# Kernel tuning notes

Hardware: AMD Instinct MI355X
Metric: run time of the kernel (lower is better)

## Reference

```python
import jax, jax.numpy as jnp
import numpy as np

B, H, W = 8, 48, 48
D_MODEL, D_STATE, SSM_RATIO, K = 192, 16, 2.0, 4
D_INNER = int(SSM_RATIO * D_MODEL)        # 384
DT_RANK = int(np.ceil(D_MODEL / 16))       # 12
EPS = 1e-6


def setup_inputs() -> dict:
    key = jax.random.key(0)
    ks = jax.random.split(key, 12)
    s = 0.02
    inp = {
        "x": jax.random.normal(ks[0], (B, H, W, D_MODEL), jnp.float32),
        "in_proj_w": s * jax.random.normal(ks[1], (2 * D_INNER, D_MODEL), jnp.float32),
        "conv_w": s * jax.random.normal(ks[2], (D_INNER, 1, 3, 3), jnp.float32),
        "conv_b": jnp.zeros((D_INNER,), jnp.float32),
        "x_proj_w": s * jax.random.normal(ks[3], (K, DT_RANK + 2 * D_STATE, D_INNER), jnp.float32),
        "dt_w": s * jax.random.normal(ks[4], (K, D_INNER, DT_RANK), jnp.float32),
        "dt_bias": 0.05 * jax.random.normal(ks[5], (K, D_INNER), jnp.float32),
        "A_logs": jnp.log(jnp.broadcast_to(jnp.arange(1, D_STATE + 1, dtype=jnp.float32), (K * D_INNER, D_STATE)).copy()),
        "Ds": jnp.ones((K * D_INNER,), jnp.float32),
        "ln_w": jnp.ones((D_INNER,), jnp.float32),
        "ln_b": jnp.zeros((D_INNER,), jnp.float32),
        "out_proj_w": s * jax.random.normal(ks[6], (D_MODEL, D_INNER), jnp.float32),
    }
    return inp


def _selective_scan(u, dt, A, Bs, Cs):
    # u, dt: (B,K,D,L); A: (K,D,N); Bs, Cs: (B,K,N,L)
    u_t = jnp.moveaxis(u, -1, 0)    # (L,B,K,D)
    dt_t = jnp.moveaxis(dt, -1, 0)  # (L,B,K,D)
    B_t = jnp.moveaxis(Bs, -1, 0)   # (L,B,K,N)
    C_t = jnp.moveaxis(Cs, -1, 0)   # (L,B,K,N)
    b = u.shape[0]
    h0 = jnp.zeros((b, K, D_INNER, D_STATE), jnp.float32)

    def step(h, inp):
        ut, dtt, bt, ct = inp
        dA = jnp.exp(dtt[..., None] * A)                       # (B,K,D,N)
        h = dA * h + (dtt * ut)[..., None] * bt[:, :, None, :]  # (B,K,D,N)
        y = jnp.einsum('bkdn,bkn->bkd', h, ct)
        return h, y

    _, ys = jax.lax.scan(step, h0, (u_t, dt_t, B_t, C_t))
    return jnp.moveaxis(ys, 0, -1)  # (B,K,D,L)


def reference(x, in_proj_w, conv_w, conv_b, x_proj_w, dt_w, dt_bias, A_logs, Ds, ln_w, ln_b, out_proj_w):
    b, h, w, _ = x.shape
    L = h * w
    # in_proj + split into x / gate z
    xz = jnp.einsum('bhwc,oc->bhwo', x, in_proj_w)
    xi, z = jnp.split(xz, 2, axis=-1)
    z = jax.nn.silu(z)
    # depthwise 3x3 conv, channel-first
    xi = jnp.transpose(xi, (0, 3, 1, 2))  # (B,Di,H,W)
    xi = jax.lax.conv_general_dilated(
        xi, conv_w, window_strides=(1, 1), padding='SAME',
        feature_group_count=D_INNER,
        dimension_numbers=('NCHW', 'OIHW', 'NCHW')) + conv_b[None, :, None, None]
    xi = jax.nn.silu(xi)
    # cross-scan: 4 directions (row-major, col-major, and their reverses)
    xr = xi.reshape(b, D_INNER, L)
    xc = jnp.transpose(xi, (0, 1, 3, 2)).reshape(b, D_INNER, L)
    xs = jnp.stack([xr, xc, jnp.flip(xr, -1), jnp.flip(xc, -1)], axis=1)  # (B,K,D,L)
    # per-direction projections
    x_dbl = jnp.einsum('bkdl,kcd->bkcl', xs, x_proj_w)  # (B,K,R+2N,L)
    dts = x_dbl[:, :, :DT_RANK]
    Bs = x_dbl[:, :, DT_RANK:DT_RANK + D_STATE]
    Cs = x_dbl[:, :, DT_RANK + D_STATE:]
    dts = jnp.einsum('bkrl,kdr->bkdl', dts, dt_w)
    A = -jnp.exp(A_logs.astype(jnp.float32)).reshape(K, D_INNER, D_STATE)
    dt = jax.nn.softplus(dts + dt_bias[None, :, :, None])
    ys = _selective_scan(xs.astype(jnp.float32), dt, A, Bs.astype(jnp.float32), Cs.astype(jnp.float32))
    ys = ys + Ds.reshape(1, K, D_INNER, 1) * xs  # skip
    # cross-merge (invert each direction, sum)
    def col2row(t):
        return jnp.transpose(t.reshape(b, D_INNER, w, h), (0, 1, 3, 2)).reshape(b, D_INNER, L)
    y = ys[:, 0] + col2row(ys[:, 1]) + jnp.flip(ys[:, 2], -1) + col2row(jnp.flip(ys[:, 3], -1))
    y = jnp.transpose(y.reshape(b, D_INNER, h, w), (0, 2, 3, 1))  # (B,H,W,Di)
    # LayerNorm over channel dim
    mu = y.mean(-1, keepdims=True)
    var = ((y - mu) ** 2).mean(-1, keepdims=True)
    y = (y - mu) / jnp.sqrt(var + EPS) * ln_w + ln_b
    # gate + out_proj
    y = y * z
    out = jnp.einsum('bhwd,od->bhwo', y, out_proj_w)
    return out.astype(x.dtype)
```

## Files before the change

kernel.cpp:

```cpp
#include <hip/hip_runtime.h>

#define BB 8
#define HH 48
#define WW2 48
#define LL 2304
#define CIN 192
#define DI 384
#define NK 4
#define RR 12
#define NS 16
#define CD 44
#define NX 176
#define MM 18432
#define NC 48
#define CL 48

typedef unsigned short u16;
typedef __attribute__((ext_vector_type(8))) short s16x8;
typedef __attribute__((ext_vector_type(4))) float f32x4;

static __device__ __forceinline__ float siluf(float x) { return x / (1.f + __expf(-x)); }

static __device__ __forceinline__ u16 f2bf(float x) {
    unsigned u = __float_as_uint(x);
    return (u16)((u + 0x7FFFu + ((u >> 16) & 1u)) >> 16);
}
static __device__ __forceinline__ float bf2f(u16 h) {
    return __uint_as_float(((unsigned)h) << 16);
}

static __device__ __forceinline__ int posmap(int k, int l) {
    switch (k & 3) {
    case 0: return l;
    case 1: { int w = l / HH; int h = l - w * HH; return h * WW2 + w; }
    case 2: return LL - 1 - l;
    default: { int j = LL - 1 - l; int w = j / HH; int h = j - w * HH; return h * WW2 + w; }
    }
}

__global__ __launch_bounds__(256) void k_cvt2(const float* __restrict__ in,
                                              u16* __restrict__ hi,
                                              u16* __restrict__ lo, int n) {
    int i = (blockIdx.x * 256 + threadIdx.x) * 4;
    if (i >= n) return;
    float4 v = *(const float4*)(in + i);
    u16 h0 = f2bf(v.x), h1 = f2bf(v.y), h2 = f2bf(v.z), h3 = f2bf(v.w);
    hi[i + 0] = h0; hi[i + 1] = h1; hi[i + 2] = h2; hi[i + 3] = h3;
    lo[i + 0] = f2bf(v.x - bf2f(h0));
    lo[i + 1] = f2bf(v.y - bf2f(h1));
    lo[i + 2] = f2bf(v.z - bf2f(h2));
    lo[i + 3] = f2bf(v.w - bf2f(h3));
}

template<int N, int K, int EPI>
__global__ __launch_bounds__(256) void k_gemm(const u16* __restrict__ Ahg,
                                              const u16* __restrict__ Alg,
                                              const u16* __restrict__ Bhg,
                                              const u16* __restrict__ Blg,
                                              float* __restrict__ O1,
                                              void* __restrict__ O2) {
    __shared__ __align__(16) u16 lds[12288];
    const int m0 = blockIdx.x << 7;
    const int n0 = blockIdx.y << 6;
    const int t = threadIdx.x;
    const int lane = t & 63;
    const int w = t >> 6;
    const int wm = w & 1, wn = w >> 1;

    f32x4 acc[4][2];
#pragma unroll
    for (int mi = 0; mi < 4; ++mi)
#pragma unroll
        for (int ni = 0; ni < 2; ++ni)
#pragma unroll
            for (int r = 0; r < 4; ++r) acc[mi][ni][r] = 0.f;

    const int rA = lane & 15;
    const int kb = (lane >> 4) << 3;

    for (int k0 = 0; k0 < K; k0 += 32) {
#pragma unroll
        for (int rep = 0; rep < 2; ++rep) {
            int q = t + (rep << 8);
            int row = q >> 2;
            int kk = (q & 3) << 3;
            size_t ga = (size_t)(m0 + row) * K + k0 + kk;
            *(uint4*)&lds[(row << 5) + kk] = *(const uint4*)(Ahg + ga);
            *(uint4*)&lds[4096 + (row << 5) + kk] = *(const uint4*)(Alg + ga);
        }
        {
            int row = t >> 2;
            int kk = (t & 3) << 3;
            int rg = n0 + row;
            if (N & 63) rg = (rg > N - 1) ? (N - 1) : rg;
            size_t gb = (size_t)rg * K + k0 + kk;
            *(uint4*)&lds[8192 + (row << 5) + kk] = *(const uint4*)(Bhg + gb);
            *(uint4*)&lds[10240 + (row << 5) + kk] = *(const uint4*)(Blg + gb);
        }
        __syncthreads();

        s16x8 bh[2], bl[2];
#pragma unroll
        for (int ni = 0; ni < 2; ++ni) {
            int c = (wn << 5) + (ni << 4) + rA;
            bh[ni] = *(const s16x8*)&lds[8192 + (c << 5) + kb];
            bl[ni] = *(const s16x8*)&lds[10240 + (c << 5) + kb];
        }
#pragma unroll
        for (int mi = 0; mi < 4; ++mi) {
            int rr = (wm << 6) + (mi << 4) + rA;
            s16x8 ah = *(const s16x8*)&lds[(rr << 5) + kb];
            s16x8 al = *(const s16x8*)&lds[4096 + (rr << 5) + kb];
#pragma unroll
            for (int ni = 0; ni < 2; ++ni) {
                acc[mi][ni] = __builtin_amdgcn_mfma_f32_16x16x32_bf16(al, bh[ni], acc[mi][ni], 0, 0, 0);
                acc[mi][ni] = __builtin_amdgcn_mfma_f32_16x16x32_bf16(ah, bl[ni], acc[mi][ni], 0, 0, 0);
                acc[mi][ni] = __builtin_amdgcn_mfma_f32_16x16x32_bf16(ah, bh[ni], acc[mi][ni], 0, 0, 0);
            }
        }
        __syncthreads();
    }

    const int rbase = (lane >> 4) << 2;
#pragma unroll
    for (int mi = 0; mi < 4; ++mi) {
#pragma unroll
        for (int ni = 0; ni < 2; ++ni) {
            int o = n0 + (wn << 5) + (ni << 4) + (lane & 15);
#pragma unroll
            for (int r = 0; r < 4; ++r) {
                int m = m0 + (wm << 6) + (mi << 4) + rbase + r;
                float v = acc[mi][ni][r];
                if (EPI == 0) {
                    if (o < DI) O1[(size_t)m * DI + o] = v;
                    else        ((u16*)O2)[(size_t)m * DI + (o - DI)] = f2bf(siluf(v));
                } else if (EPI == 1) {
                    if (o < NX) O1[(size_t)m * NX + o] = v;
                } else {
                    O1[(size_t)m * CIN + o] = v;
                }
            }
        }
    }
}

__global__ __launch_bounds__(128) void k_conv(const float* __restrict__ xi,
                                              const float* __restrict__ cw,
                                              const float* __restrict__ cb,
                                              float* __restrict__ ub,
                                              u16* __restrict__ ubh,
                                              u16* __restrict__ ubl) {
    int blk = blockIdx.x;
    int b = blk / LL, p = blk - b * LL;
    int h = p / WW2, w = p - h * WW2;
    for (int d = threadIdx.x; d < DI; d += 128) {
        float acc = cb[d];
#pragma unroll
        for (int dh = -1; dh <= 1; ++dh) {
            int hh = h + dh;
            if (hh < 0 || hh >= HH) continue;
#pragma unroll
            for (int dw = -1; dw <= 1; ++dw) {
                int ww = w + dw;
                if (ww < 0 || ww >= WW2) continue;
                acc = fmaf(cw[d * 9 + (dh + 1) * 3 + (dw + 1)],
                           xi[((size_t)b * LL + hh * WW2 + ww) * DI + d], acc);
            }
        }
        float o = siluf(acc);
        size_t idx = ((size_t)b * LL + p) * DI + d;
        ub[idx] = o;
        u16 hh2 = f2bf(o);
        ubh[idx] = hh2;
        ubl[idx] = f2bf(o - bf2f(hh2));
    }
}

static __device__ __forceinline__ void adv_p(int k, int& p, int& hh) {
    if (k == 0) { ++p; }
    else if (k == 2) { --p; }
    else if (k == 1) {
        bool wrap = (hh == HH - 1);
        hh = wrap ? 0 : hh + 1;
        p += wrap ? -(LL - 1 - HH) : WW2;
    } else {
        bool wrap = (hh == 0);
        hh = wrap ? HH - 1 : hh - 1;
        p += wrap ? (LL - 1 - HH) : -WW2;
    }
}

static __device__ __forceinline__ void init_p(int k, int l0, int& p, int& hh) {
    hh = 0;
    if (k == 0) p = l0;
    else if (k == 2) p = LL - 1 - l0;
    else if (k == 1) { int w0 = l0 / HH; hh = l0 - w0 * HH; p = hh * WW2 + w0; }
    else { int j0 = LL - 1 - l0; int w0 = j0 / HH; hh = j0 - w0 * HH; p = hh * WW2 + w0; }
}

static __device__ __forceinline__ void scan_decode(int blk, int& b, int& k, int& dblk, int& c) {
    b = blk & 7;
    int r = blk >> 3;
    c = r % NC;
    int t2 = r / NC;
    dblk = t2 % 3;
    k = t2 / 3;
}

__global__ __launch_bounds__(128) void k_scan1(const float* __restrict__ ub,
                                               const float* __restrict__ xdbl,
                                               const float* __restrict__ dt_w,
                                               const float* __restrict__ dt_bias,
                                               const float* __restrict__ A_logs,
                                               float* __restrict__ HF,
                                               float* __restrict__ SD) {
    int b, k, dblk, c;
    scan_decode(blockIdx.x, b, k, dblk, c);
    int bk = (b << 2) | k;
    int d = (dblk << 7) + threadIdx.x;
    int kd = k * DI + d;

    float dtw[RR];
#pragma unroll
    for (int r = 0; r < RR; ++r) dtw[r] = dt_w[(size_t)kd * RR + r];
    float dtb = dt_bias[kd];
    float a[NS];
    bool fast = true;
#pragma unroll
    for (int n = 0; n < NS; ++n) {
        a[n] = -__expf(A_logs[(size_t)kd * NS + n]);
        fast = fast && (fabsf(a[n] + (float)(n + 1)) < 1e-3f * (float)(n + 1));
    }
    int use_fast = __all((int)fast);

    float h[NS];
#pragma unroll
    for (int n = 0; n < NS; ++n) h[n] = 0.f;
    float sumdt = 0.f;

    const float* cb0 = xdbl + (size_t)b * LL * NX + k * CD;
    const float* ubase = ub + (size_t)b * LL * DI + d;
    const int l0 = c * CL;
    int p, hh;
    init_p(k, l0, p, hh);

    if (use_fast) {
        for (int li = 0; li < CL; ++li) {
            const float4* cp4 = (const float4*)(cb0 + (size_t)p * NX);
            float dq[12];
            *(float4*)(dq + 0) = cp4[0];
            *(float4*)(dq + 4) = cp4[1];
            *(float4*)(dq + 8) = cp4[2];
            float s = dtb;
#pragma unroll
            for (int r = 0; r < RR; ++r) s = fmaf(dtw[r], dq[r], s);
            float es = __expf(s);
            float dt = (s > 15.f) ? s : __logf(1.f + es);
            float E = __builtin_amdgcn_rcpf(1.f + es);
            sumdt += dt;
            float uv = ubase[(size_t)p * DI];
            float du = dt * uv;
            float bb2[16];
            *(float4*)(bb2 + 0)  = cp4[3];
            *(float4*)(bb2 + 4)  = cp4[4];
            *(float4*)(bb2 + 8)  = cp4[5];
            *(float4*)(bb2 + 12) = cp4[6];
            float pw = 1.f;
#pragma unroll
            for (int n = 0; n < NS; ++n) {
                pw *= E;
                h[n] = fmaf(du, bb2[n], pw * h[n]);
            }
            adv_p(k, p, hh);
        }
    } else {
        for (int li = 0; li < CL; ++li) {
            int l = l0 + li;
            int pp = posmap(k, l);
            const float* cp = cb0 + (size_t)pp * NX;
            float s = dtb;
#pragma unroll
            for (int r = 0; r < RR; ++r) s = fmaf(dtw[r], cp[r], s);
            float dt = (s > 15.f) ? s : log1pf(__expf(s));
            sumdt += dt;
            float uv = ubase[(size_t)pp * DI];
            float du = dt * uv;
#pragma unroll
            for (int n = 0; n < NS; ++n) {
                float dA = __expf(dt * a[n]);
                h[n] = fmaf(du, cp[RR + n], dA * h[n]);
            }
        }
    }
    size_t base = ((size_t)bk * NC + c);
#pragma unroll
    for (int n = 0; n < NS; ++n) HF[(base * NS + n) * DI + d] = h[n];
    SD[base * DI + d] = sumdt;
}

__global__ __launch_bounds__(256) void k_scan2(const float* __restrict__ A_logs,
                                               float* __restrict__ HF,
                                               const float* __restrict__ SD) {
    int idx = blockIdx.x * 256 + threadIdx.x;
    int bk = idx / DI;
    int d = idx - bk * DI;
    int k = bk & 3;
    int kd = k * DI + d;

    float a[NS];
    bool fast = true;
#pragma unroll
    for (int n = 0; n < NS; ++n) {
        a[n] = -__expf(A_logs[(size_t)kd * NS + n]);
        fast = fast && (fabsf(a[n] + (float)(n + 1)) < 1e-3f * (float)(n + 1));
    }
    int use_fast = __all((int)fast);

    float H[NS];
#pragma unroll
    for (int n = 0; n < NS; ++n) H[n] = 0.f;

    for (int c = 0; c < NC; ++c) {
        size_t base = ((size_t)bk * NC + c);
        float sd = SD[base * DI + d];
        if (use_fast) {
            float E = __expf(-sd);
            float pw = 1.f;
#pragma unroll
            for (int n = 0; n < NS; ++n) {
                pw *= E;
                float hf = HF[(base * NS + n) * DI + d];
                HF[(base * NS + n) * DI + d] = H[n];
                H[n] = fmaf(pw, H[n], hf);
            }
        } else {
#pragma unroll
            for (int n = 0; n < NS; ++n) {
                float dec = __expf(a[n] * sd);
                float hf = HF[(base * NS + n) * DI + d];
                HF[(base * NS + n) * DI + d] = H[n];
                H[n] = fmaf(dec, H[n], hf);
            }
        }
    }
}

__global__ __launch_bounds__(128) void k_scan3(const float* __restrict__ ub,
                                               const float* __restrict__ xdbl,
                                               const float* __restrict__ dt_w,
                                               const float* __restrict__ dt_bias,
                                               const float* __restrict__ A_logs,
                                               const float* __restrict__ Ds,
                                               const float* __restrict__ HF,
                                               float* __restrict__ ycomb) {
    int b, k, dblk, c;
    scan_decode(blockIdx.x, b, k, dblk, c);
    int bk = (b << 2) | k;
    int d = (dblk << 7) + threadIdx.x;
    int kd = k * DI + d;

    float dtw[RR];
#pragma unroll
    for (int r = 0; r < RR; ++r) dtw[r] = dt_w[(size_t)kd * RR + r];
    float dtb = dt_bias[kd];
    float dsv = Ds[kd];
    float a[NS];
    bool fast = true;
#pragma unroll
    for (int n = 0; n < NS; ++n) {
        a[n] = -__expf(A_logs[(size_t)kd * NS + n]);
        fast = fast && (fabsf(a[n] + (float)(n + 1)) < 1e-3f * (float)(n + 1));
    }
    int use_fast = __all((int)fast);

    float h[NS];
    size_t sbase = ((size_t)bk * NC + c);
#pragma unroll
    for (int n = 0; n < NS; ++n) h[n] = HF[(sbase * NS + n) * DI + d];

    const float* cb0 = xdbl + (size_t)b * LL * NX + k * CD;
    const float* ubase = ub + (size_t)b * LL * DI + d;
    float* ybase = ycomb + (size_t)b * LL * DI + d;
    const int l0 = c * CL;
    int p, hh;
    init_p(k, l0, p, hh);

    if (use_fast) {
        for (int li = 0; li < CL; ++li) {
            const float4* cp4 = (const float4*)(cb0 + (size_t)p * NX);
            float dq[12];
            *(float4*)(dq + 0) = cp4[0];
            *(float4*)(dq + 4) = cp4[1];
            *(float4*)(dq + 8) = cp4[2];
            float s = dtb;
#pragma unroll
            for (int r = 0; r < RR; ++r) s = fmaf(dtw[r], dq[r], s);
            float es = __expf(s);
            float dt = (s > 15.f) ? s : __logf(1.f + es);
            float E = __builtin_amdgcn_rcpf(1.f + es);
            float uv = ubase[(size_t)p * DI];
            float du = dt * uv;
            float bc[32];
            *(float4*)(bc + 0)  = cp4[3];
            *(float4*)(bc + 4)  = cp4[4];
            *(float4*)(bc + 8)  = cp4[5];
            *(float4*)(bc + 12) = cp4[6];
            *(float4*)(bc + 16) = cp4[7];
            *(float4*)(bc + 20) = cp4[8];
            *(float4*)(bc + 24) = cp4[9];
            *(float4*)(bc + 28) = cp4[10];
            float pw = 1.f, y = 0.f;
#pragma unroll
            for (int n = 0; n < NS; ++n) {
                pw *= E;
                h[n] = fmaf(du, bc[n], pw * h[n]);
                y = fmaf(h[n], bc[NS + n], y);
            }
            atomicAdd(ybase + (size_t)p * DI, fmaf(dsv, uv, y));
            adv_p(k, p, hh);
        }
    } else {
        for (int li = 0; li < CL; ++li) {
            int l = l0 + li;
            int pp = posmap(k, l);
            const float* cp = cb0 + (size_t)pp * NX;
            float s = dtb;
#pragma unroll
            for (int r = 0; r < RR; ++r) s = fmaf(dtw[r], cp[r], s);
            float dt = (s > 15.f) ? s : log1pf(__expf(s));
            float uv = ubase[(size_t)pp * DI];
            float du = dt * uv;
            float y = 0.f;
#pragma unroll
            for (int n = 0; n < NS; ++n) {
                float dA = __expf(dt * a[n]);
                h[n] = fmaf(du, cp[RR + n], dA * h[n]);
                y = fmaf(h[n], cp[RR + NS + n], y);
            }
            atomicAdd(ybase + (size_t)pp * DI, fmaf(dsv, uv, y));
        }
    }
}

static __device__ __forceinline__ float waveRedSum(float v) {
#pragma unroll
    for (int o = 32; o; o >>= 1) v += __shfl_down(v, o);
    return v;
}

__global__ __launch_bounds__(128) void k_lngate(const float* __restrict__ ycomb,
                                                const u16* __restrict__ zb16,
                                                const float* __restrict__ lnw,
                                                const float* __restrict__ lnb,
                                                u16* __restrict__ ylnh,
                                                u16* __restrict__ ylnl) {
    int m = blockIdx.x;
    const float* yr = ycomb + (size_t)m * DI;
    float v[3];
    float s1 = 0.f, s2 = 0.f;
#pragma unroll
    for (int i = 0; i < 3; ++i) {
        v[i] = yr[threadIdx.x + (i << 7)];
        s1 += v[i];
        s2 = fmaf(v[i], v[i], s2);
    }
    s1 = waveRedSum(s1);
    s2 = waveRedSum(s2);
    __shared__ float p1[2], p2[2];
    int wid = threadIdx.x >> 6, lane = threadIdx.x & 63;
    if (lane == 0) { p1[wid] = s1; p2[wid] = s2; }
    __syncthreads();
    float S1 = p1[0] + p1[1];
    float S2 = p2[0] + p2[1];
    float mu = S1 * (1.f / DI);
    float var = S2 * (1.f / DI) - mu * mu;
    float rstd = rsqrtf(var + 1e-6f);
#pragma unroll
    for (int i = 0; i < 3; ++i) {
        int dd = threadIdx.x + (i << 7);
        float o = ((v[i] - mu) * rstd) * lnw[dd] + lnb[dd];
        float g = o * bf2f(zb16[(size_t)m * DI + dd]);
        u16 hh = f2bf(g);
        ylnh[(size_t)m * DI + dd] = hh;
        ylnl[(size_t)m * DI + dd] = f2bf(g - bf2f(hh));
    }
}

extern "C" void kernel_launch(void* const* d_in, const int* in_sizes, int n_in,
                              void* d_out, int out_size, void* d_ws, size_t ws_size,
                              hipStream_t stream) {
    const float* x         = (const float*)d_in[0];
    const float* in_proj_w = (const float*)d_in[1];
    const float* conv_w    = (const float*)d_in[2];
    const float* conv_b    = (const float*)d_in[3];
    const float* x_proj_w  = (const float*)d_in[4];
    const float* dt_w      = (const float*)d_in[5];
    const float* dt_bias   = (const float*)d_in[6];
    const float* A_logs    = (const float*)d_in[7];
    const float* Ds        = (const float*)d_in[8];
    const float* ln_w      = (const float*)d_in[9];
    const float* ln_b      = (const float*)d_in[10];
    const float* out_proj_w= (const float*)d_in[11];
    float* out = (float*)d_out;
    float* ws  = (float*)d_ws;

    const size_t SZ = (size_t)MM * DI;
    float* xi    = ws;
    u16*   zb16  = (u16*)(ws + SZ + SZ / 2);
    float* ub    = ws + 2 * SZ;
    float* xdbl  = ws + 3 * SZ;
    float* ycomb = ws + 3 * SZ + (size_t)MM * NX;
    u16*   wpl   = (u16*)(ycomb + SZ);

    u16* wphi  = wpl;
    u16* wplo  = wpl + 147456;
    u16* xpwhi = wpl + 294912;
    u16* xpwlo = wpl + 362496;
    u16* wohi  = wpl + 430080;
    u16* wolo  = wpl + 503808;

    u16* xhi  = (u16*)ub;  u16* xlo  = xhi + (size_t)MM * CIN;
    u16* ubh  = (u16*)ycomb; u16* ubl = ubh + SZ;
    u16* ylnh = (u16*)xi;  u16* ylnl = ylnh + SZ;
    float* HF = ws;
    float* SD = ws + (size_t)BB * NK * NC * NS * DI;

    k_cvt2<<<3456, 256, 0, stream>>>(x, xhi, xlo, MM * CIN);
    k_cvt2<<<144, 256, 0, stream>>>(in_proj_w, wphi, wplo, 768 * CIN);
    k_cvt2<<<66, 256, 0, stream>>>(x_proj_w, xpwhi, xpwlo, NX * DI);
    k_cvt2<<<72, 256, 0, stream>>>(out_proj_w, wohi, wolo, CIN * DI);

    k_gemm<768, CIN, 0><<<dim3(MM / 128, 12), 256, 0, stream>>>(xhi, xlo, wphi, wplo, xi, (void*)zb16);

    k_conv<<<MM, 128, 0, stream>>>(xi, conv_w, conv_b, ub, ubh, ubl);

    k_gemm<NX, DI, 1><<<dim3(MM / 128, 3), 256, 0, stream>>>(ubh, ubl, xpwhi, xpwlo, xdbl, nullptr);

    hipMemsetAsync(ycomb, 0, SZ * sizeof(float), stream);

    const int nscan = BB * NK * 3 * NC;
    k_scan1<<<nscan, 128, 0, stream>>>(ub, xdbl, dt_w, dt_bias, A_logs, HF, SD);
    k_scan2<<<BB * NK * DI / 256, 256, 0, stream>>>(A_logs, HF, SD);
    k_scan3<<<nscan, 128, 0, stream>>>(ub, xdbl, dt_w, dt_bias, A_logs, Ds, HF, ycomb);

    k_lngate<<<MM, 128, 0, stream>>>(ycomb, zb16, ln_w, ln_b, ylnh, ylnl);

    k_gemm<CIN, DI, 2><<<dim3(MM / 128, 3), 256, 0, stream>>>(ylnh, ylnl, wohi, wolo, out, nullptr);
}
```

Before: 368.9 us.

## Fuse x hi/lo bf16 split into in_proj GEMM and widen scan blocks

The in_proj GEMM now loads fp32 x directly and splits it into bf16 hi/lo pairs while staging tiles into LDS. This removes the separate conversion kernel and the round trip of the split copies through global memory. The scan kernels also switch from 128-thread blocks over three channel slices to one 384-thread block covering all channels, cutting the block count threefold. In exchange there is conversion arithmetic inside the GEMM load loop and fewer, larger scan blocks with more register pressure per block.

```diff
diff --git a/kernel.cpp b/kernel.cpp
--- a/kernel.cpp
+++ b/kernel.cpp
@@ -52,7 +52,7 @@
     lo[i + 3] = f2bf(v.w - bf2f(h3));
 }
 
-template<int N, int K, int EPI>
+template<int N, int K, int EPI, int ACVT>
 __global__ __launch_bounds__(256) void k_gemm(const u16* __restrict__ Ahg,
                                               const u16* __restrict__ Alg,
                                               const u16* __restrict__ Bhg,
@@ -85,8 +85,24 @@
             int row = q >> 2;
             int kk = (q & 3) << 3;
             size_t ga = (size_t)(m0 + row) * K + k0 + kk;
-            *(uint4*)&lds[(row << 5) + kk] = *(const uint4*)(Ahg + ga);
-            *(uint4*)&lds[4096 + (row << 5) + kk] = *(const uint4*)(Alg + ga);
+            if (ACVT) {
+                const float* Af = (const float*)Ahg;
+                float vv[8];
+                *(float4*)(vv + 0) = *(const float4*)(Af + ga);
+                *(float4*)(vv + 4) = *(const float4*)(Af + ga + 4);
+                u16 hbuf[8], lbuf[8];
+#pragma unroll
+                for (int i = 0; i < 8; ++i) {
+                    u16 h = f2bf(vv[i]);
+                    hbuf[i] = h;
+                    lbuf[i] = f2bf(vv[i] - bf2f(h));
+                }
+                *(uint4*)&lds[(row << 5) + kk] = *(uint4*)hbuf;
+                *(uint4*)&lds[4096 + (row << 5) + kk] = *(uint4*)lbuf;
+            } else {
+                *(uint4*)&lds[(row << 5) + kk] = *(const uint4*)(Ahg + ga);
+                *(uint4*)&lds[4096 + (row << 5) + kk] = *(const uint4*)(Alg + ga);
+            }
         }
         {
             int row = t >> 2;
@@ -198,26 +214,24 @@
     else { int j0 = LL - 1 - l0; int w0 = j0 / HH; hh = j0 - w0 * HH; p = hh * WW2 + w0; }
 }
 
-static __device__ __forceinline__ void scan_decode(int blk, int& b, int& k, int& dblk, int& c) {
+static __device__ __forceinline__ void scan_decode(int blk, int& b, int& k, int& c) {
     b = blk & 7;
     int r = blk >> 3;
     c = r % NC;
-    int t2 = r / NC;
-    dblk = t2 % 3;
-    k = t2 / 3;
-}
-
-__global__ __launch_bounds__(128) void k_scan1(const float* __restrict__ ub,
+    k = r / NC;
+}
+
+__global__ __launch_bounds__(384) void k_scan1(const float* __restrict__ ub,
                                                const float* __restrict__ xdbl,
                                                const float* __restrict__ dt_w,
                                                const float* __restrict__ dt_bias,
                                                const float* __restrict__ A_logs,
                                                float* __restrict__ HF,
                                                float* __restrict__ SD) {
-    int b, k, dblk, c;
-    scan_decode(blockIdx.x, b, k, dblk, c);
+    int b, k, c;
+    scan_decode(blockIdx.x, b, k, c);
     int bk = (b << 2) | k;
-    int d = (dblk << 7) + threadIdx.x;
+    int d = threadIdx.x;
     int kd = k * DI + d;
 
     float dtw[RR];
@@ -345,7 +359,7 @@
     }
 }
 
-__global__ __launch_bounds__(128) void k_scan3(const float* __restrict__ ub,
+__global__ __launch_bounds__(384) void k_scan3(const float* __restrict__ ub,
                                                const float* __restrict__ xdbl,
                                                const float* __restrict__ dt_w,
                                                const float* __restrict__ dt_bias,
@@ -353,10 +367,10 @@
                                                const float* __restrict__ Ds,
                                                const float* __restrict__ HF,
                                                float* __restrict__ ycomb) {
-    int b, k, dblk, c;
-    scan_decode(blockIdx.x, b, k, dblk, c);
+    int b, k, c;
+    scan_decode(blockIdx.x, b, k, c);
     int bk = (b << 2) | k;
-    int d = (dblk << 7) + threadIdx.x;
+    int d = threadIdx.x;
     int kd = k * DI + d;
 
     float dtw[RR];
@@ -519,31 +533,30 @@
     u16* wohi  = wpl + 430080;
     u16* wolo  = wpl + 503808;
 
-    u16* xhi  = (u16*)ub;  u16* xlo  = xhi + (size_t)MM * CIN;
     u16* ubh  = (u16*)ycomb; u16* ubl = ubh + SZ;
     u16* ylnh = (u16*)xi;  u16* ylnl = ylnh + SZ;
     float* HF = ws;
     float* SD = ws + (size_t)BB * NK * NC * NS * DI;
 
-    k_cvt2<<<3456, 256, 0, stream>>>(x, xhi, xlo, MM * CIN);
     k_cvt2<<<144, 256, 0, stream>>>(in_proj_w, wphi, wplo, 768 * CIN);
     k_cvt2<<<66, 256, 0, stream>>>(x_proj_w, xpwhi, xpwlo, NX * DI);
     k_cvt2<<<72, 256, 0, stream>>>(out_proj_w, wohi, wolo, CIN * DI);
 
-    k_gemm<768, CIN, 0><<<dim3(MM / 128, 12), 256, 0, stream>>>(xhi, xlo, wphi, wplo, xi, (void*)zb16);
+    k_gemm<768, CIN, 0, 1><<<dim3(MM / 128, 12), 256, 0, stream>>>(
+        (const u16*)x, nullptr, wphi, wplo, xi, (void*)zb16);
 
     k_conv<<<MM, 128, 0, stream>>>(xi, conv_w, conv_b, ub, ubh, ubl);
 
-    k_gemm<NX, DI, 1><<<dim3(MM / 128, 3), 256, 0, stream>>>(ubh, ubl, xpwhi, xpwlo, xdbl, nullptr);
+    k_gemm<NX, DI, 1, 0><<<dim3(MM / 128, 3), 256, 0, stream>>>(ubh, ubl, xpwhi, xpwlo, xdbl, nullptr);
 
     hipMemsetAsync(ycomb, 0, SZ * sizeof(float), stream);
 
-    const int nscan = BB * NK * 3 * NC;
-    k_scan1<<<nscan, 128, 0, stream>>>(ub, xdbl, dt_w, dt_bias, A_logs, HF, SD);
+    const int nscan = NK * NC * 8;
+    k_scan1<<<nscan, 384, 0, stream>>>(ub, xdbl, dt_w, dt_bias, A_logs, HF, SD);
     k_scan2<<<BB * NK * DI / 256, 256, 0, stream>>>(A_logs, HF, SD);
-    k_scan3<<<nscan, 128, 0, stream>>>(ub, xdbl, dt_w, dt_bias, A_logs, Ds, HF, ycomb);
+    k_scan3<<<nscan, 384, 0, stream>>>(ub, xdbl, dt_w, dt_bias, A_logs, Ds, HF, ycomb);
 
     k_lngate<<<MM, 128, 0, stream>>>(ycomb, zb16, ln_w, ln_b, ylnh, ylnl);
 
-    k_gemm<CIN, DI, 2><<<dim3(MM / 128, 3), 256, 0, stream>>>(ylnh, ylnl, wohi, wolo, out, nullptr);
-}
+    k_gemm<CIN, DI, 2, 0><<<dim3(MM / 128, 3), 256, 0, stream>>>(ylnh, ylnl, wohi, wolo, out, nullptr);
+}
```

Measured after the change: 383.4 us. 4.0% more time.
